# Kernel optimization log

Measured on AMD Instinct MI355X. Metric: run time of the kernel, lower is better.

## Reference

```python
import jax, jax.numpy as jnp
import numpy as np

MODEL_DIM = 256
PAIR_IMPORTANCE_WEIGHT = 0.5
B, S, D = 4, 4096, MODEL_DIM


def setup_inputs() -> dict:
    key = jax.random.key(0)
    ks = jax.random.split(key, 6)
    return {
        "query": jax.random.normal(ks[0], (B, S, D), dtype=jnp.float32),
        "key": jax.random.normal(ks[1], (B, S, D), dtype=jnp.float32),
        "value": jax.random.normal(ks[2], (B, S, D), dtype=jnp.float32),
        "W_query": jax.random.normal(ks[3], (D, D), dtype=jnp.float32),
        "W_key": jax.random.normal(ks[4], (D, D), dtype=jnp.float32),
        "W_value": jax.random.normal(ks[5], (D, D), dtype=jnp.float32),
    }


def reference(query, key, value, W_query, W_key, W_value):
    # Projections: [B,S,D] @ [D,D]
    q = jnp.einsum('bsd,de->bse', query, W_query)
    k = jnp.einsum('bsd,de->bse', key, W_key)
    v = jnp.einsum('bsd,de->bse', value, W_value)
    scale = jnp.sqrt(jnp.asarray(MODEL_DIM, dtype=q.dtype))
    # Full [B,S,S] score matrix (global max forces materialization)
    scores = jnp.einsum('bqd,bkd->bqk', q, k) / scale
    s_len = scores.shape[1]
    diag_bias = jnp.eye(s_len, dtype=scores.dtype) * jnp.max(scores)
    scores = scores + PAIR_IMPORTANCE_WEIGHT * diag_bias  # broadcast over batch
    attention_weights = jax.nn.softmax(scores, axis=-1)
    output = jnp.einsum('bqk,bkd->bqd', attention_weights, v)
    return output, attention_weights
```

## Files before the change

### kernel.cpp

```cpp
#include <hip/hip_runtime.h>
#include <cstdint>
#include <cstddef>

#define BB 4
#define SS 4096
#define DD 256
#define PIW 0.5f

typedef float          f32x4  __attribute__((ext_vector_type(4)));
typedef __bf16         bf16v8 __attribute__((ext_vector_type(8)));
typedef unsigned short u16v8  __attribute__((ext_vector_type(8)));
typedef unsigned short u16v4  __attribute__((ext_vector_type(4)));

__device__ __forceinline__ f32x4 mfma_bf16(u16v8 a, u16v8 b, f32x4 c) {
    return __builtin_amdgcn_mfma_f32_16x16x32_bf16(
        __builtin_bit_cast(bf16v8, a), __builtin_bit_cast(bf16v8, b), c, 0, 0, 0);
}

__device__ __forceinline__ unsigned short f2bf(float f) {
    unsigned u = __float_as_uint(f);
    u += 0x7FFFu + ((u >> 16) & 1u);
    return (unsigned short)(u >> 16);
}
__device__ __forceinline__ float bf2f(unsigned short h) {
    return __uint_as_float(((unsigned)h) << 16);
}
__device__ __forceinline__ unsigned fenc(float x) {
    unsigned u = __float_as_uint(x);
    return (u & 0x80000000u) ? ~u : (u | 0x80000000u);
}
__device__ __forceinline__ float fdec(unsigned e) {
    return __uint_as_float((e & 0x80000000u) ? (e ^ 0x80000000u) : ~e);
}

__device__ __forceinline__ void split8(float4 x0, float4 x1, u16v8* h, u16v8* l) {
    float xs[8] = {x0.x, x0.y, x0.z, x0.w, x1.x, x1.y, x1.z, x1.w};
    #pragma unroll
    for (int e = 0; e < 8; e++) {
        unsigned short hh = f2bf(xs[e]);
        (*h)[e] = hh;
        (*l)[e] = f2bf(xs[e] - bf2f(hh));
    }
}

#define FPAD 36

__global__ __launch_bounds__(256) void proj_mfma(
    const float* __restrict__ query, const float* __restrict__ key_, const float* __restrict__ value,
    const float* __restrict__ Wq, const float* __restrict__ Wk, const float* __restrict__ Wv,
    unsigned short* __restrict__ qh, unsigned short* __restrict__ ql,
    unsigned short* __restrict__ kh, unsigned short* __restrict__ kl,
    unsigned short* __restrict__ vT, unsigned* __restrict__ gmax)
{
    const int z = blockIdx.z;
    const float* A = (z == 0) ? query : (z == 1) ? key_ : value;
    const float* W = (z == 0) ? Wq    : (z == 1) ? Wk   : Wv;
    if (z == 0 && blockIdx.x == 0 && blockIdx.y == 0 && threadIdx.x == 0)
        *gmax = 0x007FFFFFu;

    __shared__ float Af[128][FPAD];
    __shared__ float Wf[128][FPAD];

    const int tid = threadIdx.x;
    const int lane = tid & 63, w = tid >> 6;
    const int wr = (w >> 1) * 64, wc = (w & 1) * 64;
    const int m = lane & 15, qq = lane >> 4;
    const int rowBase = blockIdx.y * 128;
    const int colBase = blockIdx.x * 128;

    f32x4 acc[4][4];
    #pragma unroll
    for (int i = 0; i < 4; i++)
        #pragma unroll
        for (int j = 0; j < 4; j++)
            acc[i][j] = (f32x4){0.f, 0.f, 0.f, 0.f};

    for (int k0 = 0; k0 < DD; k0 += 32) {
        #pragma unroll
        for (int i = 0; i < 4; i++) {
            int c = tid + i * 256;
            int r = c >> 3, q8 = c & 7;
            *(float4*)&Af[r][q8 * 4] = *(const float4*)&A[(size_t)(rowBase + r) * DD + k0 + q8 * 4];
        }
        {
            int c = tid & 127, kk0 = (tid >> 7) * 16;
            #pragma unroll
            for (int kk = 0; kk < 16; kk++)
                Wf[c][kk0 + kk] = W[(size_t)(k0 + kk0 + kk) * DD + colBase + c];
        }
        __syncthreads();

        u16v8 ah[4], al[4], bh[4], bl[4];
        #pragma unroll
        for (int i = 0; i < 4; i++) {
            float4 x0 = *(const float4*)&Af[wr + i * 16 + m][qq * 8];
            float4 x1 = *(const float4*)&Af[wr + i * 16 + m][qq * 8 + 4];
            split8(x0, x1, &ah[i], &al[i]);
        }
        #pragma unroll
        for (int j = 0; j < 4; j++) {
            float4 x0 = *(const float4*)&Wf[wc + j * 16 + m][qq * 8];
            float4 x1 = *(const float4*)&Wf[wc + j * 16 + m][qq * 8 + 4];
            split8(x0, x1, &bh[j], &bl[j]);
        }
        #pragma unroll
        for (int i = 0; i < 4; i++)
            #pragma unroll
            for (int j = 0; j < 4; j++) {
                acc[i][j] = mfma_bf16(ah[i], bh[j], acc[i][j]);
                acc[i][j] = mfma_bf16(ah[i], bl[j], acc[i][j]);
                acc[i][j] = mfma_bf16(al[i], bh[j], acc[i][j]);
            }
        __syncthreads();
    }

    #pragma unroll
    for (int i = 0; i < 4; i++) {
        #pragma unroll
        for (int j = 0; j < 4; j++) {
            #pragma unroll
            for (int r = 0; r < 4; r++) {
                int gr  = rowBase + wr + i * 16 + qq * 4 + r;
                int col = colBase + wc + j * 16 + m;
                float v = acc[i][j][r];
                if (z == 2) {
                    int b2 = gr >> 12, s2 = gr & (SS - 1);
                    vT[((size_t)b2 * DD + col) * SS + s2] = f2bf(v);
                } else {
                    if (z == 0) v *= (1.0f / 16.0f);
                    unsigned short hh = f2bf(v);
                    unsigned short ll = f2bf(v - bf2f(hh));
                    size_t idx = (size_t)gr * DD + col;
                    if (z == 0) { qh[idx] = hh; ql[idx] = ll; }
                    else        { kh[idx] = hh; kl[idx] = ll; }
                }
            }
        }
    }
}

#define SPAD 40

__global__ __launch_bounds__(256) void scores_mfma(
    const unsigned short* __restrict__ qh, const unsigned short* __restrict__ ql,
    const unsigned short* __restrict__ kh, const unsigned short* __restrict__ kl,
    float* __restrict__ attn, float* __restrict__ pmax, float* __restrict__ psum,
    unsigned* __restrict__ gmax)
{
    const int b = blockIdx.z;
    const size_t boff = (size_t)b * SS * DD;
    const unsigned short* Qh = qh + boff;
    const unsigned short* Ql = ql + boff;
    const unsigned short* Kh = kh + boff;
    const unsigned short* Kl = kl + boff;
    float* C = attn + (size_t)b * SS * SS;

    __shared__ unsigned short Ah[128][SPAD];
    __shared__ unsigned short Al[128][SPAD];
    __shared__ unsigned short Bh[128][SPAD];
    __shared__ unsigned short Bl[128][SPAD];
    __shared__ float smax[128][2];
    __shared__ float ssum[128][2];
    __shared__ float red[256];

    const int tid = threadIdx.x;
    const int lane = tid & 63, w = tid >> 6;
    const int wr = (w >> 1) * 64, wc = (w & 1) * 64;
    const int m = lane & 15, qq = lane >> 4;
    const int rowBase = blockIdx.y * 128;
    const int colBase = blockIdx.x * 128;

    f32x4 acc[4][4];
    #pragma unroll
    for (int i = 0; i < 4; i++)
        #pragma unroll
        for (int j = 0; j < 4; j++)
            acc[i][j] = (f32x4){0.f, 0.f, 0.f, 0.f};

    const int chunk = (tid & 3) * 8;
    const int srow  = tid >> 2;

    for (int k0 = 0; k0 < DD; k0 += 32) {
        #pragma unroll
        for (int i = 0; i < 2; i++) {
            int r = srow + i * 64;
            size_t ga = (size_t)(rowBase + r) * DD + k0 + chunk;
            size_t gb = (size_t)(colBase + r) * DD + k0 + chunk;
            *(u16v8*)&Ah[r][chunk] = *(const u16v8*)&Qh[ga];
            *(u16v8*)&Al[r][chunk] = *(const u16v8*)&Ql[ga];
            *(u16v8*)&Bh[r][chunk] = *(const u16v8*)&Kh[gb];
            *(u16v8*)&Bl[r][chunk] = *(const u16v8*)&Kl[gb];
        }
        __syncthreads();

        const int kb = qq * 8;
        u16v8 ah[4], al[4], bh[4], bl[4];
        #pragma unroll
        for (int i = 0; i < 4; i++) {
            ah[i] = *(const u16v8*)&Ah[wr + i * 16 + m][kb];
            al[i] = *(const u16v8*)&Al[wr + i * 16 + m][kb];
            bh[i] = *(const u16v8*)&Bh[wc + i * 16 + m][kb];
            bl[i] = *(const u16v8*)&Bl[wc + i * 16 + m][kb];
        }
        #pragma unroll
        for (int i = 0; i < 4; i++)
            #pragma unroll
            for (int j = 0; j < 4; j++) {
                acc[i][j] = mfma_bf16(ah[i], bh[j], acc[i][j]);
                acc[i][j] = mfma_bf16(ah[i], bl[j], acc[i][j]);
                acc[i][j] = mfma_bf16(al[i], bh[j], acc[i][j]);
            }
        __syncthreads();
    }

    float vm_all = -INFINITY;
    #pragma unroll
    for (int i = 0; i < 4; i++) {
        #pragma unroll
        for (int r = 0; r < 4; r++) {
            int row = rowBase + wr + i * 16 + qq * 4 + r;
            float vj[4];
            float vm = -INFINITY;
            #pragma unroll
            for (int j = 0; j < 4; j++) {
                vj[j] = acc[i][j][r];
                C[(size_t)row * SS + colBase + wc + j * 16 + m] = vj[j];
                vm = fmaxf(vm, vj[j]);
            }
            #pragma unroll
            for (int o = 1; o < 16; o <<= 1)
                vm = fmaxf(vm, __shfl_xor(vm, o));
            float vs = 0.f;
            #pragma unroll
            for (int j = 0; j < 4; j++)
                vs += __expf(vj[j] - vm);
            #pragma unroll
            for (int o = 1; o < 16; o <<= 1)
                vs += __shfl_xor(vs, o);
            vm_all = fmaxf(vm_all, vm);
            if (m == 0) {
                smax[wr + i * 16 + qq * 4 + r][w & 1] = vm;
                ssum[wr + i * 16 + qq * 4 + r][w & 1] = vs;
            }
        }
    }
    red[tid] = vm_all;
    __syncthreads();
    if (tid < 128) {
        float m0 = smax[tid][0], m1 = smax[tid][1];
        float M = fmaxf(m0, m1);
        float P = ssum[tid][0] * __expf(m0 - M) + ssum[tid][1] * __expf(m1 - M);
        size_t idx = ((size_t)(b * SS + rowBase + tid)) * 32 + blockIdx.x;
        pmax[idx] = M;
        psum[idx] = P;
    }
    for (int s2 = 128; s2 > 0; s2 >>= 1) {
        if (tid < s2) red[tid] = fmaxf(red[tid], red[tid + s2]);
        __syncthreads();
    }
    if (tid == 0) atomicMax(gmax, fenc(red[0]));
}

__global__ __launch_bounds__(256) void combine_kernel(
    const float* __restrict__ pmax, const float* __restrict__ psum,
    const float* __restrict__ attn, const unsigned* __restrict__ gmax,
    float* __restrict__ rmax, float* __restrict__ rinv)
{
    const int row = blockIdx.x * 256 + threadIdx.x;
    const int b = row >> 12, i = row & (SS - 1);
    const float bias = PIW * fdec(*gmax);
    const float d = attn[(size_t)b * SS * SS + (size_t)i * SS + i];
    const float* pm = &pmax[(size_t)row * 32];
    const float* ps = &psum[(size_t)row * 32];

    float M = -INFINITY;
    #pragma unroll 8
    for (int t = 0; t < 32; t++) M = fmaxf(M, pm[t]);
    const float db = d + bias;
    const float Mrow = fmaxf(M, db);
    const int t0 = i >> 7;
    float S = 0.f;
    #pragma unroll 8
    for (int t = 0; t < 32; t++) {
        float P = ps[t];
        if (t == t0) P -= __expf(d - pm[t]);
        S += P * __expf(pm[t] - Mrow);
    }
    S += __expf(db - Mrow);
    rmax[row] = Mrow;
    rinv[row] = 1.0f / S;
}

#define APAD 72

__global__ __launch_bounds__(256) void av_fused(
    float* __restrict__ attn, const unsigned short* __restrict__ vT,
    const float* __restrict__ rmax, const float* __restrict__ rinv,
    const unsigned* __restrict__ gmax, float* __restrict__ out)
{
    const int b = blockIdx.y;
    const int rowBase = blockIdx.x * 32;
    float* A = attn + (size_t)b * SS * SS;
    const unsigned short* Bv = vT + (size_t)b * DD * SS;
    const float bias = PIW * fdec(*gmax);

    __shared__ unsigned short As[32][APAD];
    __shared__ unsigned short Bs[256][APAD];
    __shared__ float sM[32], sI[32];

    const int tid = threadIdx.x;
    const int lane = tid & 63, w = tid >> 6;
    const int m = lane & 15, qq = lane >> 4;

    if (tid < 32) {
        sM[tid] = rmax[(b << 12) + rowBase + tid];
        sI[tid] = rinv[(b << 12) + rowBase + tid];
    }
    __syncthreads();

    f32x4 acc[2][4];
    #pragma unroll
    for (int i = 0; i < 2; i++)
        #pragma unroll
        for (int j = 0; j < 4; j++)
            acc[i][j] = (f32x4){0.f, 0.f, 0.f, 0.f};

    for (int k0 = 0; k0 < SS; k0 += 64) {
        {
            const int ch = (tid & 15) * 4;
            #pragma unroll
            for (int i = 0; i < 2; i++) {
                int rr = (tid >> 4) + i * 16;
                int grow = rowBase + rr;
                size_t idx = (size_t)grow * SS + k0 + ch;
                float4 t = *(const float4*)&A[idx];
                float M = sM[rr], I = sI[rr];
                int c = k0 + ch;
                float w0 = __expf(t.x + ((c + 0 == grow) ? bias : 0.f) - M) * I;
                float w1 = __expf(t.y + ((c + 1 == grow) ? bias : 0.f) - M) * I;
                float w2 = __expf(t.z + ((c + 2 == grow) ? bias : 0.f) - M) * I;
                float w3 = __expf(t.w + ((c + 3 == grow) ? bias : 0.f) - M) * I;
                *(float4*)&A[idx] = make_float4(w0, w1, w2, w3);
                *(u16v4*)&As[rr][ch] = (u16v4){f2bf(w0), f2bf(w1), f2bf(w2), f2bf(w3)};
            }
        }
        {
            const int ch = (tid & 7) * 8;
            #pragma unroll
            for (int i = 0; i < 8; i++) {
                int r = (tid >> 3) + i * 32;
                *(u16v8*)&Bs[r][ch] = *(const u16v8*)&Bv[(size_t)r * SS + k0 + ch];
            }
        }
        __syncthreads();

        #pragma unroll
        for (int kk = 0; kk < 64; kk += 32) {
            const int kb = kk + qq * 8;
            u16v8 af[2], bf[4];
            #pragma unroll
            for (int i = 0; i < 2; i++)
                af[i] = *(const u16v8*)&As[i * 16 + m][kb];
            #pragma unroll
            for (int j = 0; j < 4; j++)
                bf[j] = *(const u16v8*)&Bs[w * 64 + j * 16 + m][kb];
            #pragma unroll
            for (int i = 0; i < 2; i++)
                #pragma unroll
                for (int j = 0; j < 4; j++)
                    acc[i][j] = mfma_bf16(af[i], bf[j], acc[i][j]);
        }
        __syncthreads();
    }

    #pragma unroll
    for (int i = 0; i < 2; i++) {
        #pragma unroll
        for (int j = 0; j < 4; j++) {
            #pragma unroll
            for (int r = 0; r < 4; r++) {
                int row = rowBase + i * 16 + qq * 4 + r;
                int col = w * 64 + j * 16 + m;
                out[((size_t)b * SS + row) * DD + col] = acc[i][j][r];
            }
        }
    }
}

extern "C" void kernel_launch(void* const* d_in, const int* in_sizes, int n_in,
                              void* d_out, int out_size, void* d_ws, size_t ws_size,
                              hipStream_t stream)
{
    const float* query = (const float*)d_in[0];
    const float* key_  = (const float*)d_in[1];
    const float* value = (const float*)d_in[2];
    const float* Wq    = (const float*)d_in[3];
    const float* Wk    = (const float*)d_in[4];
    const float* Wv    = (const float*)d_in[5];

    float* out  = (float*)d_out;
    float* attn = out + (size_t)BB * SS * DD;

    const size_t E = (size_t)BB * SS * DD;
    unsigned short* qh = (unsigned short*)d_ws;
    unsigned short* ql = qh + E;
    unsigned short* kh = ql + E;
    unsigned short* kl = kh + E;
    unsigned short* vT = kl + E;
    float* pmax = (float*)(vT + E);
    float* psum = pmax + (size_t)BB * SS * 32;
    float* rmax = psum + (size_t)BB * SS * 32;
    float* rinv = rmax + (size_t)BB * SS;
    unsigned* gmax = (unsigned*)(rinv + (size_t)BB * SS);

    proj_mfma<<<dim3(DD / 128, (BB * SS) / 128, 3), 256, 0, stream>>>(
        query, key_, value, Wq, Wk, Wv, qh, ql, kh, kl, vT, gmax);
    scores_mfma<<<dim3(SS / 128, SS / 128, BB), 256, 0, stream>>>(
        qh, ql, kh, kl, attn, pmax, psum, gmax);
    combine_kernel<<<dim3((BB * SS) / 256), 256, 0, stream>>>(
        pmax, psum, attn, gmax, rmax, rinv);
    av_fused<<<dim3(SS / 32, BB), 256, 0, stream>>>(
        attn, vT, rmax, rinv, gmax, out);
}
```

Before: 728.2 us.

## Recompute scores in AV kernel instead of round-tripping raw scores through attn

The scores kernel now produces only the per-tile row max/sum statistics and the diagonal values, so it no longer writes the full score matrix. The final kernel recomputes QK^T per 128-column tile from the split-bf16 Q/K, applies bias and normalisation, writes the attention weights once and feeds them into the AV MFMA. This removes one full write plus one read of the 256 MB score matrix, at the cost of doing the 3-pass split-bf16 QK^T matmul twice. V is also stored in a 32-column blocked transpose, and the partial stats are transposed for coalesced access in the combine kernel.

```diff
diff --git a/kernel.cpp b/kernel.cpp
--- a/kernel.cpp
+++ b/kernel.cpp
@@ -6,6 +6,7 @@
 #define SS 4096
 #define DD 256
 #define PIW 0.5f
+#define NROW (BB * SS)
 
 typedef float          f32x4  __attribute__((ext_vector_type(4)));
 typedef __bf16         bf16v8 __attribute__((ext_vector_type(8)));
@@ -50,7 +51,7 @@
     const float* __restrict__ Wq, const float* __restrict__ Wk, const float* __restrict__ Wv,
     unsigned short* __restrict__ qh, unsigned short* __restrict__ ql,
     unsigned short* __restrict__ kh, unsigned short* __restrict__ kl,
-    unsigned short* __restrict__ vT, unsigned* __restrict__ gmax)
+    unsigned short* __restrict__ vt_blk, unsigned* __restrict__ gmax)
 {
     const int z = blockIdx.z;
     const float* A = (z == 0) ? query : (z == 1) ? key_ : value;
@@ -125,7 +126,7 @@
                 float v = acc[i][j][r];
                 if (z == 2) {
                     int b2 = gr >> 12, s2 = gr & (SS - 1);
-                    vT[((size_t)b2 * DD + col) * SS + s2] = f2bf(v);
+                    vt_blk[(((size_t)b2 * 128 + (s2 >> 5)) * DD + col) * 32 + (s2 & 31)] = f2bf(v);
                 } else {
                     if (z == 0) v *= (1.0f / 16.0f);
                     unsigned short hh = f2bf(v);
@@ -141,11 +142,11 @@
 
 #define SPAD 40
 
-__global__ __launch_bounds__(256) void scores_mfma(
+__global__ __launch_bounds__(256) void scores_stats(
     const unsigned short* __restrict__ qh, const unsigned short* __restrict__ ql,
     const unsigned short* __restrict__ kh, const unsigned short* __restrict__ kl,
-    float* __restrict__ attn, float* __restrict__ pmax, float* __restrict__ psum,
-    unsigned* __restrict__ gmax)
+    float* __restrict__ pmax, float* __restrict__ psum,
+    float* __restrict__ dvec, unsigned* __restrict__ gmax)
 {
     const int b = blockIdx.z;
     const size_t boff = (size_t)b * SS * DD;
@@ -153,7 +154,6 @@
     const unsigned short* Ql = ql + boff;
     const unsigned short* Kh = kh + boff;
     const unsigned short* Kl = kl + boff;
-    float* C = attn + (size_t)b * SS * SS;
 
     __shared__ unsigned short Ah[128][SPAD];
     __shared__ unsigned short Al[128][SPAD];
@@ -213,18 +213,22 @@
         __syncthreads();
     }
 
+    if (blockIdx.x == blockIdx.y && wr == wc && (m >> 2) == qq) {
+        #pragma unroll
+        for (int i = 0; i < 4; i++)
+            dvec[b * SS + rowBase + wr + i * 16 + m] = acc[i][i][m & 3];
+    }
+
     float vm_all = -INFINITY;
     #pragma unroll
     for (int i = 0; i < 4; i++) {
         #pragma unroll
         for (int r = 0; r < 4; r++) {
-            int row = rowBase + wr + i * 16 + qq * 4 + r;
             float vj[4];
             float vm = -INFINITY;
             #pragma unroll
             for (int j = 0; j < 4; j++) {
                 vj[j] = acc[i][j][r];
-                C[(size_t)row * SS + colBase + wc + j * 16 + m] = vj[j];
                 vm = fmaxf(vm, vj[j]);
             }
             #pragma unroll
@@ -250,7 +254,7 @@
         float m0 = smax[tid][0], m1 = smax[tid][1];
         float M = fmaxf(m0, m1);
         float P = ssum[tid][0] * __expf(m0 - M) + ssum[tid][1] * __expf(m1 - M);
-        size_t idx = ((size_t)(b * SS + rowBase + tid)) * 32 + blockIdx.x;
+        size_t idx = (size_t)blockIdx.x * NROW + (b * SS + rowBase + tid);
         pmax[idx] = M;
         psum[idx] = P;
     }
@@ -263,114 +267,177 @@
 
 __global__ __launch_bounds__(256) void combine_kernel(
     const float* __restrict__ pmax, const float* __restrict__ psum,
-    const float* __restrict__ attn, const unsigned* __restrict__ gmax,
+    const float* __restrict__ dvec, const unsigned* __restrict__ gmax,
     float* __restrict__ rmax, float* __restrict__ rinv)
 {
     const int row = blockIdx.x * 256 + threadIdx.x;
-    const int b = row >> 12, i = row & (SS - 1);
+    const int i = row & (SS - 1);
     const float bias = PIW * fdec(*gmax);
-    const float d = attn[(size_t)b * SS * SS + (size_t)i * SS + i];
-    const float* pm = &pmax[(size_t)row * 32];
-    const float* ps = &psum[(size_t)row * 32];
+    const float d = dvec[row];
 
     float M = -INFINITY;
     #pragma unroll 8
-    for (int t = 0; t < 32; t++) M = fmaxf(M, pm[t]);
+    for (int t = 0; t < 32; t++) M = fmaxf(M, pmax[(size_t)t * NROW + row]);
     const float db = d + bias;
     const float Mrow = fmaxf(M, db);
     const int t0 = i >> 7;
     float S = 0.f;
     #pragma unroll 8
     for (int t = 0; t < 32; t++) {
-        float P = ps[t];
-        if (t == t0) P -= __expf(d - pm[t]);
-        S += P * __expf(pm[t] - Mrow);
+        float pm = pmax[(size_t)t * NROW + row];
+        float P  = psum[(size_t)t * NROW + row];
+        if (t == t0) P -= __expf(d - pm);
+        S += P * __expf(pm - Mrow);
     }
     S += __expf(db - Mrow);
     rmax[row] = Mrow;
     rinv[row] = 1.0f / S;
 }
 
-#define APAD 72
-
-__global__ __launch_bounds__(256) void av_fused(
-    float* __restrict__ attn, const unsigned short* __restrict__ vT,
+#define QPAD 264
+#define KPAD 72
+#define PPAD 136
+
+__global__ __launch_bounds__(256) void weights_av(
+    const unsigned short* __restrict__ qh, const unsigned short* __restrict__ ql,
+    const unsigned short* __restrict__ kh, const unsigned short* __restrict__ kl,
+    const unsigned short* __restrict__ vt_blk,
     const float* __restrict__ rmax, const float* __restrict__ rinv,
-    const unsigned* __restrict__ gmax, float* __restrict__ out)
+    const unsigned* __restrict__ gmax,
+    float* __restrict__ attn, float* __restrict__ out)
 {
     const int b = blockIdx.y;
     const int rowBase = blockIdx.x * 32;
-    float* A = attn + (size_t)b * SS * SS;
-    const unsigned short* Bv = vT + (size_t)b * DD * SS;
-    const float bias = PIW * fdec(*gmax);
-
-    __shared__ unsigned short As[32][APAD];
-    __shared__ unsigned short Bs[256][APAD];
+
+    __shared__ unsigned short Qh[32][QPAD];
+    __shared__ unsigned short Ql[32][QPAD];
+    __shared__ unsigned short Ubuf[256 * KPAD];
+    __shared__ unsigned short P[32][PPAD];
     __shared__ float sM[32], sI[32];
+
+    unsigned short* KH = Ubuf;
+    unsigned short* KL = Ubuf + 128 * KPAD;
+    unsigned short* VT = Ubuf;
 
     const int tid = threadIdx.x;
     const int lane = tid & 63, w = tid >> 6;
     const int m = lane & 15, qq = lane >> 4;
-
-    if (tid < 32) {
-        sM[tid] = rmax[(b << 12) + rowBase + tid];
-        sI[tid] = rinv[(b << 12) + rowBase + tid];
+    const float bias = PIW * fdec(*gmax);
+
+    {
+        int r = tid >> 3, c0 = (tid & 7) * 32;
+        size_t qoff = ((size_t)(b * SS + rowBase + r)) * DD + c0;
+        #pragma unroll
+        for (int u = 0; u < 4; u++) {
+            *(u16v8*)&Qh[r][c0 + u * 8] = *(const u16v8*)&qh[qoff + u * 8];
+            *(u16v8*)&Ql[r][c0 + u * 8] = *(const u16v8*)&ql[qoff + u * 8];
+        }
+        if (tid < 32) {
+            sM[tid] = rmax[b * SS + rowBase + tid];
+            sI[tid] = rinv[b * SS + rowBase + tid];
+        }
     }
     __syncthreads();
 
-    f32x4 acc[2][4];
+    f32x4 accO[2][4];
     #pragma unroll
     for (int i = 0; i < 2; i++)
         #pragma unroll
         for (int j = 0; j < 4; j++)
-            acc[i][j] = (f32x4){0.f, 0.f, 0.f, 0.f};
-
-    for (int k0 = 0; k0 < SS; k0 += 64) {
-        {
-            const int ch = (tid & 15) * 4;
-            #pragma unroll
-            for (int i = 0; i < 2; i++) {
-                int rr = (tid >> 4) + i * 16;
-                int grow = rowBase + rr;
-                size_t idx = (size_t)grow * SS + k0 + ch;
-                float4 t = *(const float4*)&A[idx];
-                float M = sM[rr], I = sI[rr];
-                int c = k0 + ch;
-                float w0 = __expf(t.x + ((c + 0 == grow) ? bias : 0.f) - M) * I;
-                float w1 = __expf(t.y + ((c + 1 == grow) ? bias : 0.f) - M) * I;
-                float w2 = __expf(t.z + ((c + 2 == grow) ? bias : 0.f) - M) * I;
-                float w3 = __expf(t.w + ((c + 3 == grow) ? bias : 0.f) - M) * I;
-                *(float4*)&A[idx] = make_float4(w0, w1, w2, w3);
-                *(u16v4*)&As[rr][ch] = (u16v4){f2bf(w0), f2bf(w1), f2bf(w2), f2bf(w3)};
-            }
-        }
-        {
-            const int ch = (tid & 7) * 8;
-            #pragma unroll
-            for (int i = 0; i < 8; i++) {
-                int r = (tid >> 3) + i * 32;
-                *(u16v8*)&Bs[r][ch] = *(const u16v8*)&Bv[(size_t)r * SS + k0 + ch];
-            }
-        }
-        __syncthreads();
-
-        #pragma unroll
-        for (int kk = 0; kk < 64; kk += 32) {
-            const int kb = kk + qq * 8;
-            u16v8 af[2], bf[4];
-            #pragma unroll
-            for (int i = 0; i < 2; i++)
-                af[i] = *(const u16v8*)&As[i * 16 + m][kb];
-            #pragma unroll
-            for (int j = 0; j < 4; j++)
-                bf[j] = *(const u16v8*)&Bs[w * 64 + j * 16 + m][kb];
-            #pragma unroll
-            for (int i = 0; i < 2; i++)
+            accO[i][j] = (f32x4){0.f, 0.f, 0.f, 0.f};
+
+    for (int ct = 0; ct < SS / 128; ct++) {
+        const int colBase = ct * 128;
+
+        f32x4 accS[2][2];
+        #pragma unroll
+        for (int i = 0; i < 2; i++)
+            #pragma unroll
+            for (int j = 0; j < 2; j++)
+                accS[i][j] = (f32x4){0.f, 0.f, 0.f, 0.f};
+
+        for (int k0 = 0; k0 < DD; k0 += 64) {
+            {
+                int kr = tid >> 1, kc = (tid & 1) * 32;
+                size_t koff = ((size_t)(b * SS + colBase + kr)) * DD + k0 + kc;
+                #pragma unroll
+                for (int u = 0; u < 4; u++) {
+                    *(u16v8*)&KH[kr * KPAD + kc + u * 8] = *(const u16v8*)&kh[koff + u * 8];
+                    *(u16v8*)&KL[kr * KPAD + kc + u * 8] = *(const u16v8*)&kl[koff + u * 8];
+                }
+            }
+            __syncthreads();
+            #pragma unroll
+            for (int kk = 0; kk < 64; kk += 32) {
+                u16v8 ah[2], al[2], bh[2], bl[2];
+                #pragma unroll
+                for (int i = 0; i < 2; i++) {
+                    ah[i] = *(const u16v8*)&Qh[i * 16 + m][k0 + kk + qq * 8];
+                    al[i] = *(const u16v8*)&Ql[i * 16 + m][k0 + kk + qq * 8];
+                }
+                #pragma unroll
+                for (int j = 0; j < 2; j++) {
+                    bh[j] = *(const u16v8*)&KH[(w * 32 + j * 16 + m) * KPAD + kk + qq * 8];
+                    bl[j] = *(const u16v8*)&KL[(w * 32 + j * 16 + m) * KPAD + kk + qq * 8];
+                }
+                #pragma unroll
+                for (int i = 0; i < 2; i++)
+                    #pragma unroll
+                    for (int j = 0; j < 2; j++) {
+                        accS[i][j] = mfma_bf16(ah[i], bh[j], accS[i][j]);
+                        accS[i][j] = mfma_bf16(ah[i], bl[j], accS[i][j]);
+                        accS[i][j] = mfma_bf16(al[i], bh[j], accS[i][j]);
+                    }
+            }
+            __syncthreads();
+        }
+
+        #pragma unroll
+        for (int i = 0; i < 2; i++) {
+            #pragma unroll
+            for (int j = 0; j < 2; j++) {
+                #pragma unroll
+                for (int rr = 0; rr < 4; rr++) {
+                    int lrow = i * 16 + qq * 4 + rr;
+                    int lcol = w * 32 + j * 16 + m;
+                    int grow = rowBase + lrow, gcol = colBase + lcol;
+                    float s = accS[i][j][rr];
+                    if (grow == gcol) s += bias;
+                    float wv = __expf(s - sM[lrow]) * sI[lrow];
+                    attn[((size_t)b * SS + grow) * SS + gcol] = wv;
+                    P[lrow][lcol] = f2bf(wv);
+                }
+            }
+        }
+        __syncthreads();
+
+        for (int kk2 = 0; kk2 < 128; kk2 += 64) {
+            #pragma unroll
+            for (int h = 0; h < 2; h++) {
+                int sblk = ct * 4 + (kk2 >> 5) + h;
+                const unsigned short* src = vt_blk + ((size_t)(b * 128 + sblk)) * DD * 32;
+                #pragma unroll
+                for (int u = 0; u < 4; u++)
+                    *(u16v8*)&VT[tid * KPAD + h * 32 + u * 8] = *(const u16v8*)&src[tid * 32 + u * 8];
+            }
+            __syncthreads();
+            #pragma unroll
+            for (int kk3 = 0; kk3 < 64; kk3 += 32) {
+                u16v8 af[2], bf[4];
+                #pragma unroll
+                for (int i = 0; i < 2; i++)
+                    af[i] = *(const u16v8*)&P[i * 16 + m][kk2 + kk3 + qq * 8];
                 #pragma unroll
                 for (int j = 0; j < 4; j++)
-                    acc[i][j] = mfma_bf16(af[i], bf[j], acc[i][j]);
-        }
-        __syncthreads();
+                    bf[j] = *(const u16v8*)&VT[(w * 64 + j * 16 + m) * KPAD + kk3 + qq * 8];
+                #pragma unroll
+                for (int i = 0; i < 2; i++)
+                    #pragma unroll
+                    for (int j = 0; j < 4; j++)
+                        accO[i][j] = mfma_bf16(af[i], bf[j], accO[i][j]);
+            }
+            __syncthreads();
+        }
     }
 
     #pragma unroll
@@ -378,10 +445,10 @@
         #pragma unroll
         for (int j = 0; j < 4; j++) {
             #pragma unroll
-            for (int r = 0; r < 4; r++) {
-                int row = rowBase + i * 16 + qq * 4 + r;
+            for (int rr = 0; rr < 4; rr++) {
+                int row = rowBase + i * 16 + qq * 4 + rr;
                 int col = w * 64 + j * 16 + m;
-                out[((size_t)b * SS + row) * DD + col] = acc[i][j][r];
+                out[((size_t)b * SS + row) * DD + col] = accO[i][j][rr];
             }
         }
     }
@@ -406,19 +473,20 @@
     unsigned short* ql = qh + E;
     unsigned short* kh = ql + E;
     unsigned short* kl = kh + E;
-    unsigned short* vT = kl + E;
-    float* pmax = (float*)(vT + E);
-    float* psum = pmax + (size_t)BB * SS * 32;
-    float* rmax = psum + (size_t)BB * SS * 32;
-    float* rinv = rmax + (size_t)BB * SS;
-    unsigned* gmax = (unsigned*)(rinv + (size_t)BB * SS);
-
-    proj_mfma<<<dim3(DD / 128, (BB * SS) / 128, 3), 256, 0, stream>>>(
-        query, key_, value, Wq, Wk, Wv, qh, ql, kh, kl, vT, gmax);
-    scores_mfma<<<dim3(SS / 128, SS / 128, BB), 256, 0, stream>>>(
-        qh, ql, kh, kl, attn, pmax, psum, gmax);
-    combine_kernel<<<dim3((BB * SS) / 256), 256, 0, stream>>>(
-        pmax, psum, attn, gmax, rmax, rinv);
-    av_fused<<<dim3(SS / 32, BB), 256, 0, stream>>>(
-        attn, vT, rmax, rinv, gmax, out);
-}
+    unsigned short* vt_blk = kl + E;
+    float* pmax = (float*)(vt_blk + E);
+    float* psum = pmax + (size_t)32 * NROW;
+    float* dvec = psum + (size_t)32 * NROW;
+    float* rmax = dvec + NROW;
+    float* rinv = rmax + NROW;
+    unsigned* gmax = (unsigned*)(rinv + NROW);
+
+    proj_mfma<<<dim3(DD / 128, NROW / 128, 3), 256, 0, stream>>>(
+        query, key_, value, Wq, Wk, Wv, qh, ql, kh, kl, vt_blk, gmax);
+    scores_stats<<<dim3(SS / 128, SS / 128, BB), 256, 0, stream>>>(
+        qh, ql, kh, kl, pmax, psum, dvec, gmax);
+    combine_kernel<<<dim3(NROW / 256), 256, 0, stream>>>(
+        pmax, psum, dvec, gmax, rmax, rinv);
+    weights_av<<<dim3(SS / 32, BB), 256, 0, stream>>>(
+        qh, ql, kh, kl, vt_blk, rmax, rinv, gmax, attn, out);
+}
```

Result: slower. 783.8 us (+7.6%).

## Double-buffer AV kernel with register prefetch, larger row tile, transpose partial stats

Applied to the files above, without the earlier changes.

Rewrites the attention-times-V kernel to process 64 rows per block with 512 threads. It double-buffers the P and V tiles in shared memory and prefetches the next chunk into registers while the MFMAs run, which removes one barrier per iteration. The per-tile partial max and sum arrays are stored tile-major so the combine kernel's reads coalesce across threads. The cost is more shared memory and registers per block, which lowers occupancy, and half as many blocks in the grid.

```diff
diff --git a/kernel.cpp b/kernel.cpp
--- a/kernel.cpp
+++ b/kernel.cpp
@@ -6,6 +6,7 @@
 #define SS 4096
 #define DD 256
 #define PIW 0.5f
+#define NROW (BB * SS)
 
 typedef float          f32x4  __attribute__((ext_vector_type(4)));
 typedef __bf16         bf16v8 __attribute__((ext_vector_type(8)));
@@ -250,7 +251,7 @@
         float m0 = smax[tid][0], m1 = smax[tid][1];
         float M = fmaxf(m0, m1);
         float P = ssum[tid][0] * __expf(m0 - M) + ssum[tid][1] * __expf(m1 - M);
-        size_t idx = ((size_t)(b * SS + rowBase + tid)) * 32 + blockIdx.x;
+        size_t idx = (size_t)blockIdx.x * NROW + (b * SS + rowBase + tid);
         pmax[idx] = M;
         psum[idx] = P;
     }
@@ -270,118 +271,132 @@
     const int b = row >> 12, i = row & (SS - 1);
     const float bias = PIW * fdec(*gmax);
     const float d = attn[(size_t)b * SS * SS + (size_t)i * SS + i];
-    const float* pm = &pmax[(size_t)row * 32];
-    const float* ps = &psum[(size_t)row * 32];
 
     float M = -INFINITY;
     #pragma unroll 8
-    for (int t = 0; t < 32; t++) M = fmaxf(M, pm[t]);
+    for (int t = 0; t < 32; t++) M = fmaxf(M, pmax[(size_t)t * NROW + row]);
     const float db = d + bias;
     const float Mrow = fmaxf(M, db);
     const int t0 = i >> 7;
     float S = 0.f;
     #pragma unroll 8
     for (int t = 0; t < 32; t++) {
-        float P = ps[t];
-        if (t == t0) P -= __expf(d - pm[t]);
-        S += P * __expf(pm[t] - Mrow);
+        float pm = pmax[(size_t)t * NROW + row];
+        float P  = psum[(size_t)t * NROW + row];
+        if (t == t0) P -= __expf(d - pm);
+        S += P * __expf(pm - Mrow);
     }
     S += __expf(db - Mrow);
     rmax[row] = Mrow;
     rinv[row] = 1.0f / S;
 }
 
-#define APAD 72
-
-__global__ __launch_bounds__(256) void av_fused(
+#define VPAD 72
+
+__global__ __launch_bounds__(512) void av_fused2(
     float* __restrict__ attn, const unsigned short* __restrict__ vT,
     const float* __restrict__ rmax, const float* __restrict__ rinv,
     const unsigned* __restrict__ gmax, float* __restrict__ out)
 {
     const int b = blockIdx.y;
-    const int rowBase = blockIdx.x * 32;
+    const int rowBase = blockIdx.x * 64;
     float* A = attn + (size_t)b * SS * SS;
     const unsigned short* Bv = vT + (size_t)b * DD * SS;
     const float bias = PIW * fdec(*gmax);
 
-    __shared__ unsigned short As[32][APAD];
-    __shared__ unsigned short Bs[256][APAD];
-    __shared__ float sM[32], sI[32];
+    __shared__ unsigned short P[2][64][VPAD];
+    __shared__ unsigned short V[2][256][VPAD];
+    __shared__ float sM[64], sI[64];
 
     const int tid = threadIdx.x;
     const int lane = tid & 63, w = tid >> 6;
     const int m = lane & 15, qq = lane >> 4;
 
-    if (tid < 32) {
-        sM[tid] = rmax[(b << 12) + rowBase + tid];
-        sI[tid] = rinv[(b << 12) + rowBase + tid];
-    }
+    if (tid < 64) {
+        sM[tid] = rmax[b * SS + rowBase + tid];
+        sI[tid] = rinv[b * SS + rowBase + tid];
+    }
+
+    const int pr = tid >> 3, pc = (tid & 7) * 8;
+    const int vr = tid >> 1, vc = (tid & 1) * 32;
+    const size_t rawRow = (size_t)(rowBase + pr) * SS;
+    const size_t vRow   = (size_t)vr * SS;
+    const int growDiag  = rowBase + pr;
+
+    float4 ra0 = *(const float4*)&A[rawRow + pc];
+    float4 ra1 = *(const float4*)&A[rawRow + pc + 4];
+    u16v8 rv[4];
+    #pragma unroll
+    for (int u = 0; u < 4; u++)
+        rv[u] = *(const u16v8*)&Bv[vRow + vc + u * 8];
     __syncthreads();
 
-    f32x4 acc[2][4];
-    #pragma unroll
-    for (int i = 0; i < 2; i++)
-        #pragma unroll
-        for (int j = 0; j < 4; j++)
+    f32x4 acc[4][2];
+    #pragma unroll
+    for (int i = 0; i < 4; i++)
+        #pragma unroll
+        for (int j = 0; j < 2; j++)
             acc[i][j] = (f32x4){0.f, 0.f, 0.f, 0.f};
 
-    for (int k0 = 0; k0 < SS; k0 += 64) {
+    const float Mr = sM[pr], Ir = sI[pr];
+
+    int cur = 0;
+    for (int ct = 0; ct < SS / 64; ct++) {
+        const int kc = ct * 64;
         {
-            const int ch = (tid & 15) * 4;
-            #pragma unroll
-            for (int i = 0; i < 2; i++) {
-                int rr = (tid >> 4) + i * 16;
-                int grow = rowBase + rr;
-                size_t idx = (size_t)grow * SS + k0 + ch;
-                float4 t = *(const float4*)&A[idx];
-                float M = sM[rr], I = sI[rr];
-                int c = k0 + ch;
-                float w0 = __expf(t.x + ((c + 0 == grow) ? bias : 0.f) - M) * I;
-                float w1 = __expf(t.y + ((c + 1 == grow) ? bias : 0.f) - M) * I;
-                float w2 = __expf(t.z + ((c + 2 == grow) ? bias : 0.f) - M) * I;
-                float w3 = __expf(t.w + ((c + 3 == grow) ? bias : 0.f) - M) * I;
-                *(float4*)&A[idx] = make_float4(w0, w1, w2, w3);
-                *(u16v4*)&As[rr][ch] = (u16v4){f2bf(w0), f2bf(w1), f2bf(w2), f2bf(w3)};
-            }
-        }
-        {
-            const int ch = (tid & 7) * 8;
-            #pragma unroll
-            for (int i = 0; i < 8; i++) {
-                int r = (tid >> 3) + i * 32;
-                *(u16v8*)&Bs[r][ch] = *(const u16v8*)&Bv[(size_t)r * SS + k0 + ch];
-            }
-        }
-        __syncthreads();
+            float xs[8] = {ra0.x, ra0.y, ra0.z, ra0.w, ra1.x, ra1.y, ra1.z, ra1.w};
+            float wv[8];
+            #pragma unroll
+            for (int e = 0; e < 8; e++) {
+                float s = xs[e] + ((kc + pc + e == growDiag) ? bias : 0.f);
+                wv[e] = __expf(s - Mr) * Ir;
+            }
+            *(float4*)&A[rawRow + kc + pc]     = make_float4(wv[0], wv[1], wv[2], wv[3]);
+            *(float4*)&A[rawRow + kc + pc + 4] = make_float4(wv[4], wv[5], wv[6], wv[7]);
+            *(u16v4*)&P[cur][pr][pc]     = (u16v4){f2bf(wv[0]), f2bf(wv[1]), f2bf(wv[2]), f2bf(wv[3])};
+            *(u16v4*)&P[cur][pr][pc + 4] = (u16v4){f2bf(wv[4]), f2bf(wv[5]), f2bf(wv[6]), f2bf(wv[7])};
+            #pragma unroll
+            for (int u = 0; u < 4; u++)
+                *(u16v8*)&V[cur][vr][vc + u * 8] = rv[u];
+        }
+        __syncthreads();
+
+        if (ct + 1 < SS / 64) {
+            const int kn = kc + 64;
+            ra0 = *(const float4*)&A[rawRow + kn + pc];
+            ra1 = *(const float4*)&A[rawRow + kn + pc + 4];
+            #pragma unroll
+            for (int u = 0; u < 4; u++)
+                rv[u] = *(const u16v8*)&Bv[vRow + kn + vc + u * 8];
+        }
 
         #pragma unroll
         for (int kk = 0; kk < 64; kk += 32) {
-            const int kb = kk + qq * 8;
-            u16v8 af[2], bf[4];
-            #pragma unroll
-            for (int i = 0; i < 2; i++)
-                af[i] = *(const u16v8*)&As[i * 16 + m][kb];
-            #pragma unroll
-            for (int j = 0; j < 4; j++)
-                bf[j] = *(const u16v8*)&Bs[w * 64 + j * 16 + m][kb];
-            #pragma unroll
-            for (int i = 0; i < 2; i++)
+            u16v8 af[4], bf[2];
+            #pragma unroll
+            for (int i = 0; i < 4; i++)
+                af[i] = *(const u16v8*)&P[cur][i * 16 + m][kk + qq * 8];
+            #pragma unroll
+            for (int j = 0; j < 2; j++)
+                bf[j] = *(const u16v8*)&V[cur][w * 32 + j * 16 + m][kk + qq * 8];
+            #pragma unroll
+            for (int i = 0; i < 4; i++)
                 #pragma unroll
-                for (int j = 0; j < 4; j++)
+                for (int j = 0; j < 2; j++)
                     acc[i][j] = mfma_bf16(af[i], bf[j], acc[i][j]);
         }
-        __syncthreads();
-    }
-
-    #pragma unroll
-    for (int i = 0; i < 2; i++) {
-        #pragma unroll
-        for (int j = 0; j < 4; j++) {
-            #pragma unroll
-            for (int r = 0; r < 4; r++) {
-                int row = rowBase + i * 16 + qq * 4 + r;
-                int col = w * 64 + j * 16 + m;
-                out[((size_t)b * SS + row) * DD + col] = acc[i][j][r];
+        cur ^= 1;
+    }
+
+    #pragma unroll
+    for (int i = 0; i < 4; i++) {
+        #pragma unroll
+        for (int j = 0; j < 2; j++) {
+            #pragma unroll
+            for (int rr = 0; rr < 4; rr++) {
+                int row = rowBase + i * 16 + qq * 4 + rr;
+                int col = w * 32 + j * 16 + m;
+                out[((size_t)b * SS + row) * DD + col] = acc[i][j][rr];
             }
         }
     }
@@ -408,17 +423,17 @@
     unsigned short* kl = kh + E;
     unsigned short* vT = kl + E;
     float* pmax = (float*)(vT + E);
-    float* psum = pmax + (size_t)BB * SS * 32;
-    float* rmax = psum + (size_t)BB * SS * 32;
-    float* rinv = rmax + (size_t)BB * SS;
-    unsigned* gmax = (unsigned*)(rinv + (size_t)BB * SS);
-
-    proj_mfma<<<dim3(DD / 128, (BB * SS) / 128, 3), 256, 0, stream>>>(
+    float* psum = pmax + (size_t)32 * NROW;
+    float* rmax = psum + (size_t)32 * NROW;
+    float* rinv = rmax + NROW;
+    unsigned* gmax = (unsigned*)(rinv + NROW);
+
+    proj_mfma<<<dim3(DD / 128, NROW / 128, 3), 256, 0, stream>>>(
         query, key_, value, Wq, Wk, Wv, qh, ql, kh, kl, vT, gmax);
     scores_mfma<<<dim3(SS / 128, SS / 128, BB), 256, 0, stream>>>(
         qh, ql, kh, kl, attn, pmax, psum, gmax);
-    combine_kernel<<<dim3((BB * SS) / 256), 256, 0, stream>>>(
+    combine_kernel<<<dim3(NROW / 256), 256, 0, stream>>>(
         pmax, psum, attn, gmax, rmax, rinv);
-    av_fused<<<dim3(SS / 32, BB), 256, 0, stream>>>(
+    av_fused2<<<dim3(SS / 64, BB), 512, 0, stream>>>(
         attn, vT, rmax, rinv, gmax, out);
 }
```

New measurement: 708.6 us. 1.03x faster.
